# Performance work log

Measured on AMD Instinct MI355X. Metric: run time of the kernel, lower is better.

The kernel has to match this reference:

```python
import jax, jax.numpy as jnp
import numpy as np

N_BINS = 18
TEMP = 0.01  # n_phases > 1e7 so effective_temperature = 0.01 (same as init default)
EPS = 1e-10  # fp16=False
PI = np.pi


def setup_inputs() -> dict:
    key = jax.random.key(0)
    k1, k2 = jax.random.split(key)
    B, C, P, A, S, T = 4, 8, 20, 30, 4, 2048
    phase = jax.random.uniform(k1, (B, C, P, S, T), jnp.float32, -PI, PI)
    amplitude = jax.random.uniform(k2, (B, C, A, S, T), jnp.float32, 0.0, 1.0)
    return {"phase": phase, "amplitude": amplitude}


def reference(phase, amplitude):
    # phase:     (B, C, Fp, S, T)
    # amplitude: (B, C, Fa, S, T)
    edges = jnp.linspace(-PI, PI, N_BINS + 1).astype(phase.dtype)
    centers = (edges[1:] + edges[:-1]) * 0.5  # (N,)

    # Soft phase binning: circular distance to each bin center, softmax over bins.
    diff = phase[..., None] - centers  # (B, C, Fp, S, T, N)
    diff = jnp.fmod(diff + PI, 2.0 * PI) - PI  # torch.fmod = truncated mod = jnp.fmod
    weights = jax.nn.softmax(-jnp.abs(diff) / TEMP, axis=-1)  # (B, C, Fp, S, T, N)

    # Amplitude-weighted histogram: contract over time.
    # dist: (B, C, Fp, Fa, S, N)
    dist = jnp.einsum('bcpstn,bcast->bcpasn', weights, amplitude)

    # Normalize to a distribution over bins, clamp, Shannon entropy.
    p = dist / (dist.sum(axis=-1, keepdims=True) + EPS)
    p = jnp.maximum(p, EPS)
    neg_entropy = (p * jnp.log(p)).sum(axis=-1)  # (B, C, Fp, Fa, S)

    mi = 1.0 + neg_entropy / jnp.log(jnp.asarray(N_BINS, dtype=p.dtype))
    # -> (B, C, S, Fp, Fa) to match torch output layout
    return jnp.transpose(mi, (0, 1, 4, 2, 3))
```

## Files before the change

kernel.cpp:

```cpp
#include <hip/hip_runtime.h>
#include <math.h>
#include <stdint.h>

#define BB 4
#define CC 8
#define PP 20
#define AA 30
#define SS 4
#define TT 2048
#define NB 18

#define TC 128
#define NCH (TT / TC)
#define PG 4
#define NPG (PP / PG)
#define WSTR 132
#define WROWS 19
#define NTH 256

#define BAR() do { asm volatile("s_waitcnt lgkmcnt(0)" ::: "memory"); \
                   __builtin_amdgcn_s_barrier(); } while (0)

typedef _Float16 half4_t __attribute__((ext_vector_type(4)));
typedef _Float16 half8_t __attribute__((ext_vector_type(8)));
typedef float f32x16 __attribute__((ext_vector_type(16)));

__device__ __forceinline__ void weight_top2(float x, int& n0, int& n1,
                                            float& w0, float& w1)
{
    const float PI_F  = 3.14159265358979323846f;
    const float INV_H = 2.8647913f;
    const float H     = 0.34906585f;
    const float INV_T = 100.0f;
    float u = (x + PI_F) * INV_H;
    n0 = (int)floorf(u);
    n0 = n0 < 0 ? 0 : (n0 > NB - 1 ? NB - 1 : n0);
    float f  = u - (float)n0 - 0.5f;
    float af = fabsf(f);
    n1 = n0 + (f >= 0.0f ? 1 : -1);
    float e;
    if (n1 < 0) {
        e = 0.0f; n1 = NB;
    } else {
        if (n1 == NB) n1 = 0;
        e = __expf(-(H * (1.0f - 2.0f * af)) * INV_T);
    }
    w0 = 1.0f / (1.0f + e);
    w1 = 1.0f - w0;
}

__global__ __launch_bounds__(NTH)
void mi_fused_kernel(const float* __restrict__ phase,
                     const float* __restrict__ amp,
                     float* __restrict__ out)
{
    __shared__ _Float16 Wl[4][WROWS * WSTR];
    __shared__ _Float16 ampT[2][AA * WSTR];

    const int tid = threadIdx.x;
    const int bid = blockIdx.x;
    const int x   = bid & 7;
    const int kk  = bid >> 3;
    const int pg  = kk % NPG;
    const int g   = x + 8 * (kk / NPG);
    const int s   = g & (SS - 1);
    const int bc  = g >> 2;

    const int wv   = tid >> 6;
    const int lane = tid & 63;
    const int mrow = lane & 31;
    const int mlh  = lane >> 5;
    const int arow = mrow < WROWS ? mrow : (WROWS - 1);
    const int brow = mrow < AA    ? mrow : (AA - 1);

    const int p = pg * PG + wv;
    const float* am  = amp   + (size_t)bc * (AA * SS * TT) + (size_t)s * TT;
    const float* phw = phase + ((size_t)(bc * PP + p) * SS + s) * TT;
    float*       op  = out   + ((size_t)(bc * SS + s) * PP + p) * AA;

    {
        uint2* wz = (uint2*)&Wl[wv][0];
        for (int i = lane; i < 627; i += 64) wz[i] = make_uint2(0u, 0u);
    }
    #pragma unroll
    for (int j = 0; j < 4; ++j) {
        int q = tid + j * 256;
        int a = q >> 5, tq = q & 31;
        if (a < AA) {
            const float4 v = *(const float4*)&am[(size_t)a * (SS * TT) + tq * 4];
            half4_t h = { (_Float16)v.x, (_Float16)v.y, (_Float16)v.z, (_Float16)v.w };
            *(half4_t*)&ampT[0][a * WSTR + tq * 4] = h;
        }
    }
    float2 ph2 = *(const float2*)&phw[lane * 2];
    BAR();

    f32x16 acc0 = {}, acc1 = {};
    int pn0[2], pn1[2];

    for (int c = 0; c < NCH; ++c) {
        const int cb = c & 1, tb = cb ^ 1;

        float2 nph2 = {};
        float4 stg[4];
        if (c + 1 < NCH) {
            nph2 = *(const float2*)&phw[(c + 1) * TC + lane * 2];
            #pragma unroll
            for (int j = 0; j < 4; ++j) {
                int q = tid + j * 256;
                int a = q >> 5, tq = q & 31;
                int ac = a < AA ? a : (AA - 1);
                stg[j] = *(const float4*)&am[(size_t)ac * (SS * TT) + (c + 1) * TC + tq * 4];
            }
        }

        #pragma unroll
        for (int j = 0; j < 2; ++j) {
            int col = lane * 2 + j;
            if (c > 0) {
                Wl[wv][pn0[j] * WSTR + col] = (_Float16)0.0f;
                Wl[wv][pn1[j] * WSTR + col] = (_Float16)0.0f;
            }
            int n0, n1; float w0, w1;
            weight_top2(j == 0 ? ph2.x : ph2.y, n0, n1, w0, w1);
            Wl[wv][n0 * WSTR + col] = (_Float16)w0;
            Wl[wv][n1 * WSTR + col] = (_Float16)w1;
            pn0[j] = n0; pn1[j] = n1;
        }

        #pragma unroll
        for (int ks = 0; ks < 8; ++ks) {
            int t0 = ks * 16 + mlh * 8;
            const _Float16* Ab = &Wl[wv][arow * WSTR + t0];
            const _Float16* Bb = &ampT[cb][brow * WSTR + t0];
            half4_t a0 = *(const half4_t*)Ab;
            half4_t a1 = *(const half4_t*)(Ab + 4);
            half4_t b0 = *(const half4_t*)Bb;
            half4_t b1 = *(const half4_t*)(Bb + 4);
            half8_t av = __builtin_shufflevector(a0, a1, 0, 1, 2, 3, 4, 5, 6, 7);
            half8_t bv = __builtin_shufflevector(b0, b1, 0, 1, 2, 3, 4, 5, 6, 7);
            if (ks & 1) acc1 = __builtin_amdgcn_mfma_f32_32x32x16_f16(av, bv, acc1, 0, 0, 0);
            else        acc0 = __builtin_amdgcn_mfma_f32_32x32x16_f16(av, bv, acc0, 0, 0, 0);
        }

        if (c + 1 < NCH) {
            #pragma unroll
            for (int j = 0; j < 4; ++j) {
                int q = tid + j * 256;
                int a = q >> 5, tq = q & 31;
                if (a < AA) {
                    half4_t h = { (_Float16)stg[j].x, (_Float16)stg[j].y,
                                  (_Float16)stg[j].z, (_Float16)stg[j].w };
                    *(half4_t*)&ampT[tb][a * WSTR + tq * 4] = h;
                }
            }
        }
        ph2 = nph2;
        BAR();
    }

    f32x16 acc = acc0 + acc1;
    float* dmp = (float*)&Wl[wv][0];
    #pragma unroll
    for (int r = 0; r < 16; ++r) {
        int row = (r & 3) + 8 * (r >> 2) + 4 * mlh;
        if (row < NB) dmp[row * 33 + mrow] = acc[r];
    }
    if (lane < AA) {
        float v[NB], tot = 0.0f;
        #pragma unroll
        for (int n = 0; n < NB; ++n) { v[n] = dmp[n * 33 + lane]; tot += v[n]; }
        float inv = 1.0f / (tot + 1e-10f);
        float ne = 0.0f;
        #pragma unroll
        for (int n = 0; n < NB; ++n) {
            float pv = fmaxf(v[n] * inv, 1e-10f);
            ne += pv * logf(pv);
        }
        op[lane] = 1.0f + ne * 0.345975362f;
    }
}

extern "C" void kernel_launch(void* const* d_in, const int* in_sizes, int n_in,
                              void* d_out, int out_size, void* d_ws, size_t ws_size,
                              hipStream_t stream)
{
    const float* phase = (const float*)d_in[0];
    const float* amp   = (const float*)d_in[1];
    float* out = (float*)d_out;
    hipLaunchKernelGGL(mi_fused_kernel, dim3(BB * CC * SS * NPG), dim3(NTH),
                       0, stream, phase, amp, out);
}
```

Before: 30.44 us.

## Deepen amplitude prefetch to two chunks ahead and simplify softmax weight math

The amplitude chunk loads now go into two register staging sets that alternate, issued two chunks ahead, with the loop manually unrolled by two so global latency has a full extra iteration to hide. The fp16 store of the next chunk into LDS now happens before the MFMA loop instead of after. The weight computation folds its constants into a single fma and uses a hardware reciprocal, and launch bounds request 4 blocks per CU. The extra staging registers raise register pressure, which the occupancy hint may constrain.

```diff
diff --git a/kernel.cpp b/kernel.cpp
--- a/kernel.cpp
+++ b/kernel.cpp
@@ -30,8 +30,6 @@
 {
     const float PI_F  = 3.14159265358979323846f;
     const float INV_H = 2.8647913f;
-    const float H     = 0.34906585f;
-    const float INV_T = 100.0f;
     float u = (x + PI_F) * INV_H;
     n0 = (int)floorf(u);
     n0 = n0 < 0 ? 0 : (n0 > NB - 1 ? NB - 1 : n0);
@@ -43,13 +41,13 @@
         e = 0.0f; n1 = NB;
     } else {
         if (n1 == NB) n1 = 0;
-        e = __expf(-(H * (1.0f - 2.0f * af)) * INV_T);
-    }
-    w0 = 1.0f / (1.0f + e);
+        e = __expf(fmaf(af, 69.81317008f, -34.90658504f));
+    }
+    w0 = __builtin_amdgcn_rcpf(1.0f + e);
     w1 = 1.0f - w0;
 }
 
-__global__ __launch_bounds__(NTH)
+__global__ __launch_bounds__(NTH, 4)
 void mi_fused_kernel(const float* __restrict__ phase,
                      const float* __restrict__ amp,
                      float* __restrict__ out)
@@ -92,72 +90,84 @@
             *(half4_t*)&ampT[0][a * WSTR + tq * 4] = h;
         }
     }
+    float4 stgA[4], stgB[4];
+    #pragma unroll
+    for (int j = 0; j < 4; ++j) {
+        int q = tid + j * 256;
+        int a = q >> 5, tq = q & 31;
+        int ac = a < AA ? a : (AA - 1);
+        stgA[j] = *(const float4*)&am[(size_t)ac * (SS * TT) + TC + tq * 4];
+    }
     float2 ph2 = *(const float2*)&phw[lane * 2];
     BAR();
 
     f32x16 acc0 = {}, acc1 = {};
     int pn0[2], pn1[2];
 
-    for (int c = 0; c < NCH; ++c) {
-        const int cb = c & 1, tb = cb ^ 1;
-
-        float2 nph2 = {};
-        float4 stg[4];
-        if (c + 1 < NCH) {
-            nph2 = *(const float2*)&phw[(c + 1) * TC + lane * 2];
-            #pragma unroll
-            for (int j = 0; j < 4; ++j) {
-                int q = tid + j * 256;
-                int a = q >> 5, tq = q & 31;
-                int ac = a < AA ? a : (AA - 1);
-                stg[j] = *(const float4*)&am[(size_t)ac * (SS * TT) + (c + 1) * TC + tq * 4];
-            }
-        }
-
-        #pragma unroll
-        for (int j = 0; j < 2; ++j) {
-            int col = lane * 2 + j;
-            if (c > 0) {
-                Wl[wv][pn0[j] * WSTR + col] = (_Float16)0.0f;
-                Wl[wv][pn1[j] * WSTR + col] = (_Float16)0.0f;
-            }
-            int n0, n1; float w0, w1;
-            weight_top2(j == 0 ? ph2.x : ph2.y, n0, n1, w0, w1);
-            Wl[wv][n0 * WSTR + col] = (_Float16)w0;
-            Wl[wv][n1 * WSTR + col] = (_Float16)w1;
-            pn0[j] = n0; pn1[j] = n1;
-        }
-
-        #pragma unroll
-        for (int ks = 0; ks < 8; ++ks) {
-            int t0 = ks * 16 + mlh * 8;
-            const _Float16* Ab = &Wl[wv][arow * WSTR + t0];
-            const _Float16* Bb = &ampT[cb][brow * WSTR + t0];
-            half4_t a0 = *(const half4_t*)Ab;
-            half4_t a1 = *(const half4_t*)(Ab + 4);
-            half4_t b0 = *(const half4_t*)Bb;
-            half4_t b1 = *(const half4_t*)(Bb + 4);
-            half8_t av = __builtin_shufflevector(a0, a1, 0, 1, 2, 3, 4, 5, 6, 7);
-            half8_t bv = __builtin_shufflevector(b0, b1, 0, 1, 2, 3, 4, 5, 6, 7);
-            if (ks & 1) acc1 = __builtin_amdgcn_mfma_f32_32x32x16_f16(av, bv, acc1, 0, 0, 0);
-            else        acc0 = __builtin_amdgcn_mfma_f32_32x32x16_f16(av, bv, acc0, 0, 0, 0);
-        }
-
-        if (c + 1 < NCH) {
-            #pragma unroll
-            for (int j = 0; j < 4; ++j) {
-                int q = tid + j * 256;
-                int a = q >> 5, tq = q & 31;
-                if (a < AA) {
-                    half4_t h = { (_Float16)stg[j].x, (_Float16)stg[j].y,
-                                  (_Float16)stg[j].z, (_Float16)stg[j].w };
-                    *(half4_t*)&ampT[tb][a * WSTR + tq * 4] = h;
-                }
-            }
-        }
-        ph2 = nph2;
-        BAR();
-    }
+    #define STEP(C, SIN, SOUT)                                                 \
+    {                                                                          \
+        if ((C) + 2 < NCH) {                                                   \
+            _Pragma("unroll")                                                  \
+            for (int j = 0; j < 4; ++j) {                                      \
+                int q = tid + j * 256;                                         \
+                int a = q >> 5, tq = q & 31;                                   \
+                int ac = a < AA ? a : (AA - 1);                                \
+                SOUT[j] = *(const float4*)&am[(size_t)ac * (SS * TT)           \
+                                              + ((C) + 2) * TC + tq * 4];      \
+            }                                                                  \
+        }                                                                      \
+        float2 nph2 = {};                                                      \
+        if ((C) + 1 < NCH)                                                     \
+            nph2 = *(const float2*)&phw[((C) + 1) * TC + lane * 2];            \
+        if ((C) + 1 < NCH) {      \
+            _Pragma("unroll")                                                  \
+            for (int j = 0; j < 4; ++j) {                                      \
+                int q = tid + j * 256;                                         \
+                int a = q >> 5, tq = q & 31;                                   \
+                if (a < AA) {                                                  \
+                    half4_t h = { (_Float16)SIN[j].x, (_Float16)SIN[j].y,      \
+                                  (_Float16)SIN[j].z, (_Float16)SIN[j].w };    \
+                    *(half4_t*)&ampT[((C) + 1) & 1][a * WSTR + tq * 4] = h;    \
+                }                                                              \
+            }                                                                  \
+        }                                                                      \
+        _Pragma("unroll")                                                      \
+        for (int j = 0; j < 2; ++j) {                                          \
+            int col = lane * 2 + j;                                            \
+            if ((C) > 0) {                                                     \
+                Wl[wv][pn0[j] * WSTR + col] = (_Float16)0.0f;                  \
+                Wl[wv][pn1[j] * WSTR + col] = (_Float16)0.0f;                  \
+            }                                                                  \
+            int n0, n1; float w0, w1;                                          \
+            weight_top2(j == 0 ? ph2.x : ph2.y, n0, n1, w0, w1);               \
+            Wl[wv][n0 * WSTR + col] = (_Float16)w0;                            \
+            Wl[wv][n1 * WSTR + col] = (_Float16)w1;                            \
+            pn0[j] = n0; pn1[j] = n1;                                          \
+        }                                                                      \
+        _Pragma("unroll")                                                      \
+        for (int ks = 0; ks < 8; ++ks) {                                       \
+            int t0 = ks * 16 + mlh * 8;                                        \
+            const _Float16* Ab = &Wl[wv][arow * WSTR + t0];                    \
+            const _Float16* Bb = &ampT[(C) & 1][brow * WSTR + t0];             \
+            half4_t a0 = *(const half4_t*)Ab;                                  \
+            half4_t a1 = *(const half4_t*)(Ab + 4);                            \
+            half4_t b0 = *(const half4_t*)Bb;                                  \
+            half4_t b1 = *(const half4_t*)(Bb + 4);                            \
+            half8_t av = __builtin_shufflevector(a0, a1, 0, 1, 2, 3, 4, 5, 6, 7); \
+            half8_t bv = __builtin_shufflevector(b0, b1, 0, 1, 2, 3, 4, 5, 6, 7); \
+            if (ks & 1) acc1 = __builtin_amdgcn_mfma_f32_32x32x16_f16(av, bv, acc1, 0, 0, 0); \
+            else        acc0 = __builtin_amdgcn_mfma_f32_32x32x16_f16(av, bv, acc0, 0, 0, 0); \
+        }                                                                      \
+        ph2 = nph2;                                                            \
+        BAR();                                                                 \
+    }
+
+    #pragma unroll 1
+    for (int c = 0; c < NCH; c += 2) {
+        STEP(c,     stgA, stgB);
+        STEP(c + 1, stgB, stgA);
+    }
+    #undef STEP
 
     f32x16 acc = acc0 + acc1;
     float* dmp = (float*)&Wl[wv][0];
```

New measurement: 32.49 us. +6.8%, slower.
